# Performance work log

Measured on AMD Instinct MI355X. Metric: run time of the kernel, lower is better.

The kernel has to match this reference:

```python
import jax, jax.numpy as jnp
import numpy as np

B, T, C = 2, 2048, 1024
H = 16
D = C // H  # head_dim = 64
ROPE_BASE = 10000.0


def _rope_tables(seq_len, dim, dtype=jnp.float32):
    inv_freq = 1.0 / (ROPE_BASE ** (jnp.arange(0, dim, 2, dtype=jnp.float32) / dim))
    t = jnp.arange(seq_len, dtype=jnp.float32)
    freqs = jnp.einsum('i,j->ij', t, inv_freq)          # [T, D/2]
    emb = jnp.concatenate([freqs, freqs], axis=-1)      # [T, D]
    return jnp.cos(emb).astype(dtype), jnp.sin(emb).astype(dtype)


def _rotate_half(x):
    x1, x2 = jnp.split(x, 2, axis=-1)
    return jnp.concatenate([-x2, x1], axis=-1)


def setup_inputs() -> dict:
    key = jax.random.key(0)
    ks = jax.random.split(key, 9)
    s = 0.02
    return {
        'x': jax.random.normal(ks[0], (B, T, C), jnp.float32),
        'Wq': jax.random.normal(ks[1], (C, C), jnp.float32) * s,
        'bq': jax.random.normal(ks[2], (C,), jnp.float32) * s,
        'Wk': jax.random.normal(ks[3], (C, C), jnp.float32) * s,
        'bk': jax.random.normal(ks[4], (C,), jnp.float32) * s,
        'Wv': jax.random.normal(ks[5], (C, C), jnp.float32) * s,
        'bv': jax.random.normal(ks[6], (C,), jnp.float32) * s,
        'Wo': jax.random.normal(ks[7], (C, C), jnp.float32) * s,
        'bo': jax.random.normal(ks[8], (C,), jnp.float32) * s,
    }


def reference(x, Wq, bq, Wk, bk, Wv, bv, Wo, bo):
    b, t, c = x.shape
    q = x @ Wq.T + bq
    k = x @ Wk.T + bk
    v = x @ Wv.T + bv
    # [B, H, T, D]
    q = q.reshape(b, t, H, D).transpose(0, 2, 1, 3)
    k = k.reshape(b, t, H, D).transpose(0, 2, 1, 3)
    v = v.reshape(b, t, H, D).transpose(0, 2, 1, 3)
    cos, sin = _rope_tables(t, D, x.dtype)  # [T, D]
    q = q * cos + _rotate_half(q) * sin
    k = k * cos + _rotate_half(k) * sin
    scale = 1.0 / jnp.sqrt(jnp.array(D, x.dtype))
    scores = jnp.einsum('bhqd,bhkd->bhqk', q, k) * scale
    causal = jnp.triu(jnp.full((t, t), -jnp.inf, dtype=x.dtype), k=1)
    scores = scores + causal
    attn = jax.nn.softmax(scores, axis=-1)
    out = jnp.einsum('bhqk,bhkd->bhqd', attn, v)
    out = out.transpose(0, 2, 1, 3).reshape(b, t, c)
    return out @ Wo.T + bo
```

## Files before the change

kernel.cpp:

```cpp
#include <hip/hip_runtime.h>


typedef unsigned short u16;
typedef unsigned int u32;
typedef __bf16 bf16_t;
typedef bf16_t bf16x8 __attribute__((ext_vector_type(8)));
typedef short s16x4 __attribute__((ext_vector_type(4)));
typedef float f32x4 __attribute__((ext_vector_type(4)));
typedef float f32x16 __attribute__((ext_vector_type(16)));

#if __has_builtin(__builtin_amdgcn_mfma_f32_32x32x8bf16_1k)
#define HAVE_MFMA328 1
#else
#define HAVE_MFMA328 0
#endif

#if __has_builtin(__builtin_amdgcn_exp2f)
#define EXP2(x) __builtin_amdgcn_exp2f(x)
#else
#define EXP2(x) exp2f(x)
#endif

__device__ __forceinline__ u16 f2bf(float f) {
  union { float f; unsigned u; } v; v.f = f;
  return (u16)((v.u + 0x7FFFu + ((v.u >> 16) & 1u)) >> 16);
}

__device__ __forceinline__ void gload_lds16(const void* g, void* l) {
  __builtin_amdgcn_global_load_lds(
      (const __attribute__((address_space(1))) void*)g,
      (__attribute__((address_space(3))) void*)l, 16, 0, 0);
}

__global__ __launch_bounds__(256) void prep_kernel(
    const float* __restrict__ x, const float* __restrict__ Wq,
    const float* __restrict__ Wk, const float* __restrict__ Wv,
    const float* __restrict__ Wo, const float* __restrict__ bq,
    const float* __restrict__ bk, const float* __restrict__ bv,
    u16* __restrict__ xb, u16* __restrict__ Wqkvo, float* __restrict__ tab,
    float* __restrict__ bcat) {
  const int bid = blockIdx.x, tid = threadIdx.x;
  if (bid < 4096) {
    int i = bid * 256 + tid;
    float4 f = ((const float4*)x)[i];
    ushort4 o;
    o.x = f2bf(f.x); o.y = f2bf(f.y); o.z = f2bf(f.z); o.w = f2bf(f.w);
    ((ushort4*)xb)[i] = o;
  } else if (bid < 8192) {
    int wsel = (bid - 4096) >> 10;
    int i = ((bid - 4096) & 1023) * 256 + tid;
    const float* in = (wsel == 0) ? Wq : (wsel == 1) ? Wk : (wsel == 2) ? Wv : Wo;
    float4 f = ((const float4*)in)[i];
    ushort4 o;
    o.x = f2bf(f.x); o.y = f2bf(f.y); o.z = f2bf(f.z); o.w = f2bf(f.w);
    ((ushort4*)(Wqkvo + (size_t)wsel * 1048576))[i] = o;
  } else if (bid < 8448) {
    int idx = (bid - 8192) * 256 + tid;
    int t = idx >> 5, i = idx & 31;
    float freq = EXP2(-(float)i * 0.41524101185092034f);
    float a = (float)t * freq;
    tab[t * 64 + i] = cosf(a);
    tab[t * 64 + 32 + i] = sinf(a);
  } else {
    int j = (bid - 8448) * 256 + tid;
    float v = (j < 1024) ? bq[j] : (j < 2048) ? bk[j - 1024] : bv[j - 2048];
    bcat[j] = v;
  }
}

__device__ __forceinline__ void stage256(const u16* __restrict__ A,
                                         const u16* __restrict__ Bt,
                                         int m0, int n0, int k0,
                                         u16* lA, u16* lB, int tid) {
#pragma unroll
  for (int r = 0; r < 4; ++r) {
    int ch = r * 512 + tid;
    int row = ch >> 3, s = ch & 7;
    gload_lds16(A + (size_t)(m0 + row) * 1024 + k0 + ((s ^ (row & 7)) << 3),
                lA + ch * 8);
  }
#pragma unroll
  for (int r = 0; r < 4; ++r) {
    int ch = r * 512 + tid;
    int row = ch >> 3, s = ch & 7;
    gload_lds16(Bt + (size_t)(n0 + row) * 1024 + k0 + ((s ^ (row & 7)) << 3),
                lB + ch * 8);
  }
}

__device__ __forceinline__ void gemm256_db(const u16* __restrict__ A,
                                           const u16* __restrict__ Bt,
                                           int m0, int n0, u16* lA, u16* lB,
                                           f32x4 acc[8][4]) {
  const int tid = threadIdx.x;
  const int l = tid & 63;
  const int wid = tid >> 6, wr = wid >> 2, wc = wid & 3;

#pragma unroll
  for (int m = 0; m < 8; ++m)
#pragma unroll
    for (int n = 0; n < 4; ++n)
      acc[m][n] = (f32x4){0.f, 0.f, 0.f, 0.f};

  stage256(A, Bt, m0, n0, 0, lA, lB, tid);

  int cur = 0;
  for (int t = 0; t < 16; ++t) {
    if (t + 1 < 16) {
      stage256(A, Bt, m0, n0, (t + 1) * 64, lA + (cur ^ 1) * 16384,
               lB + (cur ^ 1) * 16384, tid);
      asm volatile("s_waitcnt vmcnt(8)" ::: "memory");
    } else {
      asm volatile("s_waitcnt vmcnt(0)" ::: "memory");
    }
    __builtin_amdgcn_s_barrier();

    const u16* pA = lA + cur * 16384;
    const u16* pB = lB + cur * 16384;
#pragma unroll
    for (int kk = 0; kk < 2; ++kk) {
      bf16x8 af[8], bf[4];
#pragma unroll
      for (int m = 0; m < 8; ++m) {
        int row = wr * 128 + m * 16 + (l & 15);
        int slot = (kk * 4 + (l >> 4)) ^ (row & 7);
        af[m] = *(const bf16x8*)(pA + row * 64 + slot * 8);
      }
#pragma unroll
      for (int n = 0; n < 4; ++n) {
        int row = wc * 64 + n * 16 + (l & 15);
        int slot = (kk * 4 + (l >> 4)) ^ (row & 7);
        bf[n] = *(const bf16x8*)(pB + row * 64 + slot * 8);
      }
#pragma unroll
      for (int m = 0; m < 8; ++m)
#pragma unroll
        for (int n = 0; n < 4; ++n)
          acc[m][n] =
              __builtin_amdgcn_mfma_f32_16x16x32_bf16(af[m], bf[n], acc[m][n], 0, 0, 0);
    }
    __builtin_amdgcn_s_barrier();
    cur ^= 1;
  }
}

__device__ __forceinline__ void stage128(const u16* __restrict__ A,
                                         const u16* __restrict__ Bt,
                                         int m0, int n0, int k0,
                                         u16* lA, u16* lB, int tid) {
#pragma unroll
  for (int r = 0; r < 4; ++r) {
    int ch = r * 256 + tid;
    int row = ch >> 3, s = ch & 7;
    gload_lds16(A + (size_t)(m0 + row) * 1024 + k0 + ((s ^ (row & 7)) << 3),
                lA + ch * 8);
  }
#pragma unroll
  for (int r = 0; r < 4; ++r) {
    int ch = r * 256 + tid;
    int row = ch >> 3, s = ch & 7;
    gload_lds16(Bt + (size_t)(n0 + row) * 1024 + k0 + ((s ^ (row & 7)) << 3),
                lB + ch * 8);
  }
}

__device__ __forceinline__ void gemm128_db(const u16* __restrict__ A,
                                           const u16* __restrict__ Bt,
                                           int m0, int n0, u16* lA, u16* lB,
                                           f32x4 acc[4][4]) {
  const int tid = threadIdx.x;
  const int l = tid & 63;
  const int wr = tid >> 7, wc = (tid >> 6) & 1;

#pragma unroll
  for (int m = 0; m < 4; ++m)
#pragma unroll
    for (int n = 0; n < 4; ++n)
      acc[m][n] = (f32x4){0.f, 0.f, 0.f, 0.f};

  stage128(A, Bt, m0, n0, 0, lA, lB, tid);

  int cur = 0;
  for (int t = 0; t < 16; ++t) {
    if (t + 1 < 16) {
      stage128(A, Bt, m0, n0, (t + 1) * 64, lA + (cur ^ 1) * 8192,
               lB + (cur ^ 1) * 8192, tid);
      asm volatile("s_waitcnt vmcnt(8)" ::: "memory");
    } else {
      asm volatile("s_waitcnt vmcnt(0)" ::: "memory");
    }
    __builtin_amdgcn_s_barrier();

    const u16* pA = lA + cur * 8192;
    const u16* pB = lB + cur * 8192;
#pragma unroll
    for (int kk = 0; kk < 2; ++kk) {
      bf16x8 af[4], bf[4];
#pragma unroll
      for (int m = 0; m < 4; ++m) {
        int row = wr * 64 + m * 16 + (l & 15);
        int slot = (kk * 4 + (l >> 4)) ^ (row & 7);
        af[m] = *(const bf16x8*)(pA + row * 64 + slot * 8);
      }
#pragma unroll
      for (int n = 0; n < 4; ++n) {
        int row = wc * 64 + n * 16 + (l & 15);
        int slot = (kk * 4 + (l >> 4)) ^ (row & 7);
        bf[n] = *(const bf16x8*)(pB + row * 64 + slot * 8);
      }
#pragma unroll
      for (int m = 0; m < 4; ++m)
#pragma unroll
        for (int n = 0; n < 4; ++n)
          acc[m][n] =
              __builtin_amdgcn_mfma_f32_16x16x32_bf16(af[m], bf[n], acc[m][n], 0, 0, 0);
    }
    __builtin_amdgcn_s_barrier();
    cur ^= 1;
  }
}

__global__ __launch_bounds__(512, 2) void qkv_kernel(
    const u16* __restrict__ xb, const u16* __restrict__ Wqkv,
    const float* __restrict__ bcat, const float* __restrict__ tab,
    u16* __restrict__ Q, u16* __restrict__ Kr, u16* __restrict__ Vt) {
  __shared__ __align__(16) u16 lds[65536];
  const int bid = blockIdx.x;
  const int xcd = bid & 7, t24 = bid >> 3;
  const int lm = t24 / 6, ln = t24 % 6;
  const int m0 = (((xcd >> 1) << 2) + lm) * 256;
  const int n0 = (((xcd & 1) * 6) + ln) * 256;

  f32x4 acc[8][4];
  gemm256_db(xb, Wqkv, m0, n0, lds, lds + 32768, acc);

  const int tid = threadIdx.x, l = tid & 63;
  const int wid = tid >> 6, wr = wid >> 2, wc = wid & 3;
  const int gcb = n0 + wc * 64;
  const int z = gcb >> 10, h = (gcb >> 6) & 15;
  const int grb = m0 + wr * 128;
  const int b2 = grb >> 11, t0 = grb & 2047;
  u16* myl = lds + wid * 8192;

  if (z < 2) {
#pragma unroll
    for (int m = 0; m < 8; ++m)
#pragma unroll
      for (int n = 0; n < 4; ++n)
#pragma unroll
        for (int jr = 0; jr < 4; ++jr) {
          int tl = m * 16 + ((l >> 4) << 2) + jr;
          int d = n * 16 + (l & 15);
          int t = t0 + tl;
          float val = acc[m][n][jr] + bcat[gcb + d];
          float p = acc[m][n ^ 2][jr] + bcat[gcb + (d ^ 32)];
          float cs = tab[t * 64 + (d & 31)];
          float sn = tab[t * 64 + 32 + (d & 31)];
          float rot = (d < 32) ? -p : p;
          float o = val * cs + rot * sn;
          if (z == 0) o *= 0.18033688011112042f;
          myl[tl * 64 + d] = f2bf(o);
        }
    asm volatile("s_waitcnt lgkmcnt(0)" ::: "memory");
    u16* dstb = ((z == 0) ? Q : Kr) + (((size_t)(b2 * 16 + h) << 11) + t0) * 64;
#pragma unroll
    for (int i = 0; i < 16; ++i) {
      int c = i * 64 + l;
      *(bf16x8*)(dstb + c * 8) = *(const bf16x8*)(myl + c * 8);
    }
  } else {
#pragma unroll
    for (int m = 0; m < 8; ++m)
#pragma unroll
      for (int n = 0; n < 4; ++n)
#pragma unroll
        for (int jr = 0; jr < 4; ++jr) {
          int tl = m * 16 + ((l >> 4) << 2) + jr;
          int d = n * 16 + (l & 15);
          float val = acc[m][n][jr] + bcat[gcb + d];
          myl[d * 128 + (tl ^ ((d & 7) << 4))] = f2bf(val);
        }
    asm volatile("s_waitcnt lgkmcnt(0)" ::: "memory");
#pragma unroll
    for (int i = 0; i < 16; ++i) {
      int c = i * 64 + l;
      int d = c >> 4, off = (c & 15) * 8;
      bf16x8 v = *(const bf16x8*)(myl + d * 128 + (off ^ ((d & 7) << 4)));
      *(bf16x8*)(Vt + (((size_t)((b2 * 16 + h) * 64 + d)) << 11) + t0 + off) = v;
    }
  }
}

__global__ __launch_bounds__(256, 2) void outproj_kernel(
    const u16* __restrict__ attn, const u16* __restrict__ Wob,
    const float* __restrict__ bo, float* __restrict__ out) {
  __shared__ __align__(16) u16 lA[2 * 128 * 64];
  __shared__ __align__(16) u16 lB[2 * 128 * 64];
  const int bid = blockIdx.x;
  const int tile = (bid & 7) * 32 + (bid >> 3);
  const int m0 = (tile >> 3) * 128, n0 = (tile & 7) * 128;
  f32x4 acc[4][4];
  gemm128_db(attn, Wob, m0, n0, lA, lB, acc);
  const int tid = threadIdx.x, l = tid & 63;
  const int wr = tid >> 7, wc = (tid >> 6) & 1;
#pragma unroll
  for (int m = 0; m < 4; ++m)
#pragma unroll
    for (int n = 0; n < 4; ++n)
#pragma unroll
      for (int jr = 0; jr < 4; ++jr) {
        int gr = m0 + wr * 64 + m * 16 + ((l >> 4) << 2) + jr;
        int gc = n0 + wc * 64 + n * 16 + (l & 15);
        out[(size_t)gr * 1024 + gc] = acc[m][n][jr] + bo[gc];
      }
}

__global__ __launch_bounds__(512) void attn_kernel(const u16* __restrict__ Q,
                                                   const u16* __restrict__ K,
                                                   const u16* __restrict__ Vt,
                                                   u16* __restrict__ out) {
  __shared__ __align__(16) u16 lK[2][2][4096];
  __shared__ __align__(16) u16 lV[2][2][4096];
  const int tid = threadIdx.x, l = tid & 63;
  const int w8 = tid >> 6;
  const int grp = w8 >> 2, w = w8 & 3;
  const int gtid = tid & 255;
  const int n = blockIdx.x;
  const int xcd = n & 7, j = n >> 3;
  const int bh = xcd * 4 + (j & 3);
  const int ji = j >> 2;
  const int qb = (ji < 8) ? (15 - ji) : (ji - 8);
  const int b = bh >> 4, h = bh & 15;
  const int lq = l & 31, hl = l >> 5;
  const int q0w = qb * 128 + w * 32;
  const int qg = q0w + lq;

  const u16* qbase = Q + ((((size_t)bh) << 11) + qg) * 64 + hl * 8;
  bf16x8 qf[4];
#pragma unroll
  for (int kd = 0; kd < 4; ++kd) qf[kd] = *(const bf16x8*)(qbase + kd * 16);

  const f32x16 z16 = {0.f, 0.f, 0.f, 0.f, 0.f, 0.f, 0.f, 0.f,
                      0.f, 0.f, 0.f, 0.f, 0.f, 0.f, 0.f, 0.f};
  f32x16 oacc[2];
  oacc[0] = z16; oacc[1] = z16;
  float mi = -1e30f, li = 0.f;

  const int nth = qb + 1;
  const int tb = grp * nth;

#define STAGE_KV(it_, buf_)                                                        \
  {                                                                                \
    _Pragma("unroll") for (int r = 0; r < 2; ++r) {                                \
      int ch = r * 256 + gtid;                                                     \
      int row = ch >> 3, s = ch & 7;                                               \
      gload_lds16(                                                                 \
          K + ((((size_t)bh) << 11) + (it_) * 64 + row) * 64 + ((s ^ (row & 7)) << 3), \
          &lK[grp][buf_][0] + ch * 8);                                             \
    }                                                                              \
    _Pragma("unroll") for (int r = 0; r < 2; ++r) {                                \
      int ch = r * 256 + gtid;                                                     \
      int row = ch >> 3, s = ch & 7;                                               \
      gload_lds16(                                                                 \
          Vt + ((((size_t)bh) * 64 + row) << 11) + (it_) * 64 + ((s ^ (row & 7)) << 3), \
          &lV[grp][buf_][0] + ch * 8);                                             \
    }                                                                              \
  }

  STAGE_KV(tb, 0);
  int cur = 0;

  for (int it = 0; it < nth; ++it) {
    const int tile = tb + it;
    const int kv0 = tile * 64;
    if (it + 1 < nth) {
      STAGE_KV(tile + 1, cur ^ 1);
      asm volatile("s_waitcnt vmcnt(4)" ::: "memory");
    } else {
      asm volatile("s_waitcnt vmcnt(0)" ::: "memory");
    }
    __builtin_amdgcn_s_barrier();

    const bool active = (kv0 <= q0w + 31);
    if (active) {
      const u16* pK = &lK[grp][cur][0];
      const u16* pV = &lV[grp][cur][0];

      f32x16 sacc[2];
      sacc[0] = z16; sacc[1] = z16;
#pragma unroll
      for (int g = 0; g < 2; ++g) {
        int row = g * 32 + lq;
        int sw = row & 7;
#pragma unroll
        for (int kd = 0; kd < 4; ++kd) {
          bf16x8 kf = *(const bf16x8*)(pK + row * 64 + (((kd * 2 + hl) ^ sw) << 3));
          sacc[g] = __builtin_amdgcn_mfma_f32_32x32x16_bf16(kf, qf[kd], sacc[g], 0, 0, 0);
        }
      }

      if (kv0 + 63 > q0w) {
#pragma unroll
        for (int g = 0; g < 2; ++g)
#pragma unroll
          for (int r = 0; r < 16; ++r) {
            int kv = kv0 + g * 32 + (r & 3) + ((r >> 2) << 3) + hl * 4;
            if (kv > qg) sacc[g][r] = -1e30f;
          }
      }

      float mx[16];
#pragma unroll
      for (int r = 0; r < 16; ++r) mx[r] = fmaxf(sacc[0][r], sacc[1][r]);
#pragma unroll
      for (int s = 8; s > 0; s >>= 1)
#pragma unroll
        for (int r = 0; r < s; ++r) mx[r] = fmaxf(mx[r], mx[r + s]);
      float mt = fmaxf(mx[0], __shfl_xor(mx[0], 32, 64));

      if (!__all(mt <= mi + 8.0f)) {
        float mn = fmaxf(mi, mt);
        float al = EXP2(mi - mn);
        mi = mn;
#pragma unroll
        for (int dblk = 0; dblk < 2; ++dblk)
#pragma unroll
          for (int r = 0; r < 16; ++r) oacc[dblk][r] *= al;
        li *= al;
      }
#pragma unroll
      for (int g = 0; g < 2; ++g)
#pragma unroll
        for (int r = 0; r < 16; ++r) sacc[g][r] = EXP2(sacc[g][r] - mi);
      float sm[16];
#pragma unroll
      for (int r = 0; r < 16; ++r) sm[r] = sacc[0][r] + sacc[1][r];
#pragma unroll
      for (int s = 8; s > 0; s >>= 1)
#pragma unroll
        for (int r = 0; r < s; ++r) sm[r] += sm[r + s];
      float rs = sm[0] + __shfl_xor(sm[0], 32, 64);
      li += rs;

      u32 pw[2][8];
#pragma unroll
      for (int g = 0; g < 2; ++g)
#pragma unroll
        for (int i = 0; i < 8; ++i) {
          union { bf16_t h2[2]; u32 u; } pk;
          pk.h2[0] = (bf16_t)sacc[g][2 * i];
          pk.h2[1] = (bf16_t)sacc[g][2 * i + 1];
          pw[g][i] = pk.u;
        }

#if HAVE_MFMA328
#pragma unroll
      for (int dblk = 0; dblk < 2; ++dblk) {
        int row = dblk * 32 + lq;
        int sw = row & 7;
#pragma unroll
        for (int g = 0; g < 2; ++g)
#pragma unroll
          for (int sb = 0; sb < 4; ++sb) {
            int s = g * 4 + sb;
            s16x4 vf = *(const s16x4*)(pV + row * 64 + ((s ^ sw) << 3) + (hl << 2));
            union { u32 u[2]; s16x4 v; } bb;
            bb.u[0] = pw[g][2 * sb];
            bb.u[1] = pw[g][2 * sb + 1];
            oacc[dblk] = __builtin_amdgcn_mfma_f32_32x32x8bf16_1k(vf, bb.v,
                                                                 oacc[dblk], 0, 0, 0);
          }
      }
#else
      u32 px[2][8];
#pragma unroll
      for (int g = 0; g < 2; ++g)
#pragma unroll
        for (int i = 0; i < 8; ++i)
          px[g][i] = (u32)__shfl_xor((int)pw[g][i], 32, 64);

      bf16x8 pfrag[4];
#pragma unroll
      for (int km = 0; km < 4; ++km) {
        const int g = km >> 1, o = (km & 1) * 4;
        union { u32 u[4]; bf16x8 v; } f;
        f.u[0] = hl ? px[g][o + 2] : pw[g][o + 0];
        f.u[1] = hl ? px[g][o + 3] : pw[g][o + 1];
        f.u[2] = hl ? pw[g][o + 2] : px[g][o + 0];
        f.u[3] = hl ? pw[g][o + 3] : px[g][o + 1];
        pfrag[km] = f.v;
      }
#pragma unroll
      for (int dblk = 0; dblk < 2; ++dblk) {
        int row = dblk * 32 + lq;
        int sw = row & 7;
#pragma unroll
        for (int km = 0; km < 4; ++km) {
          bf16x8 vf = *(const bf16x8*)(pV + row * 64 + (((km * 2 + hl) ^ sw) << 3));
          oacc[dblk] = __builtin_amdgcn_mfma_f32_32x32x16_bf16(vf, pfrag[km],
                                                              oacc[dblk], 0, 0, 0);
        }
      }
#endif
    }
    __builtin_amdgcn_s_barrier();
    cur ^= 1;
  }
#undef STAGE_KV

  float* cb = (float*)&lK[0][0][0];
  float* ml = (float*)&lV[0][0][0];
  if (grp == 1) {
    float* myo = cb + w * 2048;
#pragma unroll
    for (int dblk = 0; dblk < 2; ++dblk)
#pragma unroll
      for (int r = 0; r < 16; ++r) {
        int d = dblk * 32 + (r & 3) + ((r >> 2) << 3) + hl * 4;
        myo[d * 32 + lq] = oacc[dblk][r];
      }
    ml[w * 64 + lq] = mi;
    ml[w * 64 + 32 + lq] = li;
  }
  asm volatile("s_waitcnt lgkmcnt(0)" ::: "memory");
  __builtin_amdgcn_s_barrier();

  if (grp == 0) {
    const float m1 = ml[w * 64 + lq];
    const float l1 = ml[w * 64 + 32 + lq];
    const float* po = cb + w * 2048;
    const float m = fmaxf(mi, m1);
    const float w0 = EXP2(mi - m), w1 = EXP2(m1 - m);
    const float inv = 1.0f / (li * w0 + l1 * w1);
    const size_t rowbase = ((size_t)(b * 2048 + qg)) * 1024 + h * 64;
#pragma unroll
    for (int dblk = 0; dblk < 2; ++dblk)
#pragma unroll
      for (int g4 = 0; g4 < 4; ++g4) {
        ushort4 st;
#pragma unroll
        for (int jj = 0; jj < 4; ++jj) {
          int r = g4 * 4 + jj;
          int d = dblk * 32 + g4 * 8 + hl * 4 + jj;
          float o = (oacc[dblk][r] * w0 + po[d * 32 + lq] * w1) * inv;
          ((u16*)&st)[jj] = f2bf(o);
        }
        *(ushort4*)((u16*)out + rowbase + dblk * 32 + g4 * 8 + hl * 4) = st;
      }
  }
}

extern "C" void kernel_launch(void* const* d_in, const int* in_sizes, int n_in,
                              void* d_out, int out_size, void* d_ws, size_t ws_size,
                              hipStream_t stream) {
  const float* x  = (const float*)d_in[0];
  const float* Wq = (const float*)d_in[1];
  const float* bq = (const float*)d_in[2];
  const float* Wk = (const float*)d_in[3];
  const float* bk = (const float*)d_in[4];
  const float* Wv = (const float*)d_in[5];
  const float* bv = (const float*)d_in[6];
  const float* Wo = (const float*)d_in[7];
  const float* bo = (const float*)d_in[8];
  float* out = (float*)d_out;

  char* ws = (char*)d_ws;
  u16* xb    = (u16*)(ws);
  u16* Wqkvo = (u16*)(ws + (8ull << 20));
  u16* Wob   = Wqkvo + 3 * 1048576;
  u16* Qr  = (u16*)(ws + (16ull << 20));
  u16* Kr  = (u16*)(ws + (24ull << 20));
  u16* Vt  = (u16*)(ws + (32ull << 20));
  u16* At  = (u16*)(ws + (40ull << 20));
  float* tab  = (float*)(ws + (48ull << 20));
  float* bcat = (float*)(ws + (48ull << 20) + (512ull << 10));

  prep_kernel<<<dim3(8460), dim3(256), 0, stream>>>(x, Wq, Wk, Wv, Wo, bq, bk, bv,
                                                    xb, Wqkvo, tab, bcat);
  qkv_kernel<<<dim3(192), dim3(512), 0, stream>>>(xb, Wqkvo, bcat, tab,
                                                  Qr, Kr, Vt);
  attn_kernel<<<dim3(512), dim3(512), 0, stream>>>(Qr, Kr, Vt, At);
  outproj_kernel<<<dim3(256), dim3(256), 0, stream>>>(At, Wob, bo, out);
}
```

Measured before the change: 114.1 us.

## Stage two KV tiles per pipeline step in attention kernel

The attention loop now loads and processes K/V tiles in pairs, so each double-buffered stage holds two 64-row tiles. This halves the number of barrier and wait pairs per KV sweep and lets more loads stay in flight. In exchange, LDS use doubles to 128KB per block, which may reduce occupancy. An odd tile count also triggers a clamped redundant load that is then skipped.

```diff
diff --git a/kernel.cpp b/kernel.cpp
--- a/kernel.cpp
+++ b/kernel.cpp
@@ -319,8 +319,8 @@
                                                    const u16* __restrict__ K,
                                                    const u16* __restrict__ Vt,
                                                    u16* __restrict__ out) {
-  __shared__ __align__(16) u16 lK[2][2][4096];
-  __shared__ __align__(16) u16 lV[2][2][4096];
+  __shared__ __align__(16) u16 lK[2][2][8192];
+  __shared__ __align__(16) u16 lV[2][2][8192];
   const int tid = threadIdx.x, l = tid & 63;
   const int w8 = tid >> 6;
   const int grp = w8 >> 2, w = w8 & 3;
@@ -348,165 +348,174 @@
 
   const int nth = qb + 1;
   const int tb = grp * nth;
-
-#define STAGE_KV(it_, buf_)                                                        \
+  const int np = (nth + 1) >> 1;
+  const int tmax = 2 * qb + 1;
+
+#define STAGE_PAIR(pair_, buf_)                                                    \
   {                                                                                \
-    _Pragma("unroll") for (int r = 0; r < 2; ++r) {                                \
-      int ch = r * 256 + gtid;                                                     \
-      int row = ch >> 3, s = ch & 7;                                               \
-      gload_lds16(                                                                 \
-          K + ((((size_t)bh) << 11) + (it_) * 64 + row) * 64 + ((s ^ (row & 7)) << 3), \
-          &lK[grp][buf_][0] + ch * 8);                                             \
+    _Pragma("unroll") for (int sub = 0; sub < 2; ++sub) {                          \
+      int ts_ = tb + 2 * (pair_) + sub;                                            \
+      if (ts_ > tmax) ts_ = tmax;                                                  \
+      _Pragma("unroll") for (int r = 0; r < 2; ++r) {                              \
+        int ch = r * 256 + gtid;                                                   \
+        int row = ch >> 3, s = ch & 7;                                             \
+        gload_lds16(                                                               \
+            K + ((((size_t)bh) << 11) + ts_ * 64 + row) * 64 + ((s ^ (row & 7)) << 3), \
+            &lK[grp][buf_][sub * 4096] + ch * 8);                                  \
+      }                                                                            \
+      _Pragma("unroll") for (int r = 0; r < 2; ++r) {                              \
+        int ch = r * 256 + gtid;                                                   \
+        int row = ch >> 3, s = ch & 7;                                             \
+        gload_lds16(                                                               \
+            Vt + ((((size_t)bh) * 64 + row) << 11) + ts_ * 64 + ((s ^ (row & 7)) << 3), \
+            &lV[grp][buf_][sub * 4096] + ch * 8);                                  \
+      }                                                                            \
     }                                                                              \
-    _Pragma("unroll") for (int r = 0; r < 2; ++r) {                                \
-      int ch = r * 256 + gtid;                                                     \
-      int row = ch >> 3, s = ch & 7;                                               \
-      gload_lds16(                                                                 \
-          Vt + ((((size_t)bh) * 64 + row) << 11) + (it_) * 64 + ((s ^ (row & 7)) << 3), \
-          &lV[grp][buf_][0] + ch * 8);                                             \
-    }                                                                              \
-  }
-
-  STAGE_KV(tb, 0);
+  }
+
+  STAGE_PAIR(0, 0);
   int cur = 0;
 
-  for (int it = 0; it < nth; ++it) {
-    const int tile = tb + it;
-    const int kv0 = tile * 64;
-    if (it + 1 < nth) {
-      STAGE_KV(tile + 1, cur ^ 1);
-      asm volatile("s_waitcnt vmcnt(4)" ::: "memory");
+  for (int p = 0; p < np; ++p) {
+    if (p + 1 < np) {
+      STAGE_PAIR(p + 1, cur ^ 1);
+      asm volatile("s_waitcnt vmcnt(8)" ::: "memory");
     } else {
       asm volatile("s_waitcnt vmcnt(0)" ::: "memory");
     }
     __builtin_amdgcn_s_barrier();
 
-    const bool active = (kv0 <= q0w + 31);
-    if (active) {
-      const u16* pK = &lK[grp][cur][0];
-      const u16* pV = &lV[grp][cur][0];
-
-      f32x16 sacc[2];
-      sacc[0] = z16; sacc[1] = z16;
-#pragma unroll
-      for (int g = 0; g < 2; ++g) {
-        int row = g * 32 + lq;
-        int sw = row & 7;
-#pragma unroll
-        for (int kd = 0; kd < 4; ++kd) {
-          bf16x8 kf = *(const bf16x8*)(pK + row * 64 + (((kd * 2 + hl) ^ sw) << 3));
-          sacc[g] = __builtin_amdgcn_mfma_f32_32x32x16_bf16(kf, qf[kd], sacc[g], 0, 0, 0);
-        }
-      }
-
-      if (kv0 + 63 > q0w) {
+#pragma unroll
+    for (int sub = 0; sub < 2; ++sub) {
+      const int lt = 2 * p + sub;
+      const int kv0 = (tb + lt) * 64;
+      const bool active = (lt < nth) && (kv0 <= q0w + 31);
+      if (active) {
+        const u16* pK = &lK[grp][cur][sub * 4096];
+        const u16* pV = &lV[grp][cur][sub * 4096];
+
+        f32x16 sacc[2];
+        sacc[0] = z16; sacc[1] = z16;
+#pragma unroll
+        for (int g = 0; g < 2; ++g) {
+          int row = g * 32 + lq;
+          int sw = row & 7;
+#pragma unroll
+          for (int kd = 0; kd < 4; ++kd) {
+            bf16x8 kf = *(const bf16x8*)(pK + row * 64 + (((kd * 2 + hl) ^ sw) << 3));
+            sacc[g] = __builtin_amdgcn_mfma_f32_32x32x16_bf16(kf, qf[kd], sacc[g], 0, 0, 0);
+          }
+        }
+
+        if (kv0 + 63 > q0w) {
+#pragma unroll
+          for (int g = 0; g < 2; ++g)
+#pragma unroll
+            for (int r = 0; r < 16; ++r) {
+              int kv = kv0 + g * 32 + (r & 3) + ((r >> 2) << 3) + hl * 4;
+              if (kv > qg) sacc[g][r] = -1e30f;
+            }
+        }
+
+        float mx[16];
+#pragma unroll
+        for (int r = 0; r < 16; ++r) mx[r] = fmaxf(sacc[0][r], sacc[1][r]);
+#pragma unroll
+        for (int s = 8; s > 0; s >>= 1)
+#pragma unroll
+          for (int r = 0; r < s; ++r) mx[r] = fmaxf(mx[r], mx[r + s]);
+        float mt = fmaxf(mx[0], __shfl_xor(mx[0], 32, 64));
+
+        if (!__all(mt <= mi + 8.0f)) {
+          float mn = fmaxf(mi, mt);
+          float al = EXP2(mi - mn);
+          mi = mn;
+#pragma unroll
+          for (int dblk = 0; dblk < 2; ++dblk)
+#pragma unroll
+            for (int r = 0; r < 16; ++r) oacc[dblk][r] *= al;
+          li *= al;
+        }
 #pragma unroll
         for (int g = 0; g < 2; ++g)
 #pragma unroll
-          for (int r = 0; r < 16; ++r) {
-            int kv = kv0 + g * 32 + (r & 3) + ((r >> 2) << 3) + hl * 4;
-            if (kv > qg) sacc[g][r] = -1e30f;
+          for (int r = 0; r < 16; ++r) sacc[g][r] = EXP2(sacc[g][r] - mi);
+        float sm[16];
+#pragma unroll
+        for (int r = 0; r < 16; ++r) sm[r] = sacc[0][r] + sacc[1][r];
+#pragma unroll
+        for (int s = 8; s > 0; s >>= 1)
+#pragma unroll
+          for (int r = 0; r < s; ++r) sm[r] += sm[r + s];
+        float rs = sm[0] + __shfl_xor(sm[0], 32, 64);
+        li += rs;
+
+        u32 pw[2][8];
+#pragma unroll
+        for (int g = 0; g < 2; ++g)
+#pragma unroll
+          for (int i = 0; i < 8; ++i) {
+            union { bf16_t h2[2]; u32 u; } pk;
+            pk.h2[0] = (bf16_t)sacc[g][2 * i];
+            pk.h2[1] = (bf16_t)sacc[g][2 * i + 1];
+            pw[g][i] = pk.u;
           }
-      }
-
-      float mx[16];
-#pragma unroll
-      for (int r = 0; r < 16; ++r) mx[r] = fmaxf(sacc[0][r], sacc[1][r]);
-#pragma unroll
-      for (int s = 8; s > 0; s >>= 1)
-#pragma unroll
-        for (int r = 0; r < s; ++r) mx[r] = fmaxf(mx[r], mx[r + s]);
-      float mt = fmaxf(mx[0], __shfl_xor(mx[0], 32, 64));
-
-      if (!__all(mt <= mi + 8.0f)) {
-        float mn = fmaxf(mi, mt);
-        float al = EXP2(mi - mn);
-        mi = mn;
-#pragma unroll
-        for (int dblk = 0; dblk < 2; ++dblk)
-#pragma unroll
-          for (int r = 0; r < 16; ++r) oacc[dblk][r] *= al;
-        li *= al;
-      }
-#pragma unroll
-      for (int g = 0; g < 2; ++g)
-#pragma unroll
-        for (int r = 0; r < 16; ++r) sacc[g][r] = EXP2(sacc[g][r] - mi);
-      float sm[16];
-#pragma unroll
-      for (int r = 0; r < 16; ++r) sm[r] = sacc[0][r] + sacc[1][r];
-#pragma unroll
-      for (int s = 8; s > 0; s >>= 1)
-#pragma unroll
-        for (int r = 0; r < s; ++r) sm[r] += sm[r + s];
-      float rs = sm[0] + __shfl_xor(sm[0], 32, 64);
-      li += rs;
-
-      u32 pw[2][8];
-#pragma unroll
-      for (int g = 0; g < 2; ++g)
-#pragma unroll
-        for (int i = 0; i < 8; ++i) {
-          union { bf16_t h2[2]; u32 u; } pk;
-          pk.h2[0] = (bf16_t)sacc[g][2 * i];
-          pk.h2[1] = (bf16_t)sacc[g][2 * i + 1];
-          pw[g][i] = pk.u;
-        }
 
 #if HAVE_MFMA328
 #pragma unroll
-      for (int dblk = 0; dblk < 2; ++dblk) {
-        int row = dblk * 32 + lq;
-        int sw = row & 7;
+        for (int dblk = 0; dblk < 2; ++dblk) {
+          int row = dblk * 32 + lq;
+          int sw = row & 7;
+#pragma unroll
+          for (int g = 0; g < 2; ++g)
+#pragma unroll
+            for (int sb = 0; sb < 4; ++sb) {
+              int s = g * 4 + sb;
+              s16x4 vf = *(const s16x4*)(pV + row * 64 + ((s ^ sw) << 3) + (hl << 2));
+              union { u32 u[2]; s16x4 v; } bb;
+              bb.u[0] = pw[g][2 * sb];
+              bb.u[1] = pw[g][2 * sb + 1];
+              oacc[dblk] = __builtin_amdgcn_mfma_f32_32x32x8bf16_1k(vf, bb.v,
+                                                                   oacc[dblk], 0, 0, 0);
+            }
+        }
+#else
+        u32 px[2][8];
 #pragma unroll
         for (int g = 0; g < 2; ++g)
 #pragma unroll
-          for (int sb = 0; sb < 4; ++sb) {
-            int s = g * 4 + sb;
-            s16x4 vf = *(const s16x4*)(pV + row * 64 + ((s ^ sw) << 3) + (hl << 2));
-            union { u32 u[2]; s16x4 v; } bb;
-            bb.u[0] = pw[g][2 * sb];
-            bb.u[1] = pw[g][2 * sb + 1];
-            oacc[dblk] = __builtin_amdgcn_mfma_f32_32x32x8bf16_1k(vf, bb.v,
-                                                                 oacc[dblk], 0, 0, 0);
+          for (int i = 0; i < 8; ++i)
+            px[g][i] = (u32)__shfl_xor((int)pw[g][i], 32, 64);
+
+        bf16x8 pfrag[4];
+#pragma unroll
+        for (int km = 0; km < 4; ++km) {
+          const int g = km >> 1, o = (km & 1) * 4;
+          union { u32 u[4]; bf16x8 v; } f;
+          f.u[0] = hl ? px[g][o + 2] : pw[g][o + 0];
+          f.u[1] = hl ? px[g][o + 3] : pw[g][o + 1];
+          f.u[2] = hl ? pw[g][o + 2] : px[g][o + 0];
+          f.u[3] = hl ? pw[g][o + 3] : px[g][o + 1];
+          pfrag[km] = f.v;
+        }
+#pragma unroll
+        for (int dblk = 0; dblk < 2; ++dblk) {
+          int row = dblk * 32 + lq;
+          int sw = row & 7;
+#pragma unroll
+          for (int km = 0; km < 4; ++km) {
+            bf16x8 vf = *(const bf16x8*)(pV + row * 64 + (((km * 2 + hl) ^ sw) << 3));
+            oacc[dblk] = __builtin_amdgcn_mfma_f32_32x32x16_bf16(vf, pfrag[km],
+                                                                oacc[dblk], 0, 0, 0);
           }
-      }
-#else
-      u32 px[2][8];
-#pragma unroll
-      for (int g = 0; g < 2; ++g)
-#pragma unroll
-        for (int i = 0; i < 8; ++i)
-          px[g][i] = (u32)__shfl_xor((int)pw[g][i], 32, 64);
-
-      bf16x8 pfrag[4];
-#pragma unroll
-      for (int km = 0; km < 4; ++km) {
-        const int g = km >> 1, o = (km & 1) * 4;
-        union { u32 u[4]; bf16x8 v; } f;
-        f.u[0] = hl ? px[g][o + 2] : pw[g][o + 0];
-        f.u[1] = hl ? px[g][o + 3] : pw[g][o + 1];
-        f.u[2] = hl ? pw[g][o + 2] : px[g][o + 0];
-        f.u[3] = hl ? pw[g][o + 3] : px[g][o + 1];
-        pfrag[km] = f.v;
-      }
-#pragma unroll
-      for (int dblk = 0; dblk < 2; ++dblk) {
-        int row = dblk * 32 + lq;
-        int sw = row & 7;
-#pragma unroll
-        for (int km = 0; km < 4; ++km) {
-          bf16x8 vf = *(const bf16x8*)(pV + row * 64 + (((km * 2 + hl) ^ sw) << 3));
-          oacc[dblk] = __builtin_amdgcn_mfma_f32_32x32x16_bf16(vf, pfrag[km],
-                                                              oacc[dblk], 0, 0, 0);
-        }
-      }
+        }
 #endif
+      }
     }
     __builtin_amdgcn_s_barrier();
     cur ^= 1;
   }
-#undef STAGE_KV
+#undef STAGE_PAIR
 
   float* cb = (float*)&lK[0][0][0];
   float* ml = (float*)&lV[0][0][0];
```

Result: no change. 113.1 us (median of 2 runs) (-0.9%).
